# Kernel optimization log

Hardware: AMD Instinct MI355X
Metric: run time of the kernel (lower is better)

Reference implementation:

```python
import jax, jax.numpy as jnp
import numpy as np

B, C, P, T, H = 4, 256, 1024, 64, 8
D = C // H
SCALE = float(np.sqrt(D * T))


def setup_inputs() -> dict:
    key = jax.random.key(0)
    ks = jax.random.split(key, 7)
    s = 1.0 / np.sqrt(C)
    return {
        "x": jax.random.normal(ks[0], (B, C, P, T), dtype=jnp.float32),
        "Wk": jax.random.uniform(ks[1], (C, C), dtype=jnp.float32, minval=-s, maxval=s),
        "bk": jax.random.uniform(ks[2], (C,), dtype=jnp.float32, minval=-s, maxval=s),
        "Wq": jax.random.uniform(ks[3], (C, C), dtype=jnp.float32, minval=-s, maxval=s),
        "bq": jax.random.uniform(ks[4], (C,), dtype=jnp.float32, minval=-s, maxval=s),
        "Wv": jax.random.uniform(ks[5], (C, C), dtype=jnp.float32, minval=-s, maxval=s),
        "bv": jax.random.uniform(ks[6], (C,), dtype=jnp.float32, minval=-s, maxval=s),
    }


def _proj_split(x, W, b):
    # 1x1 conv == channel-mixing linear; then split heads: b (h d) p t -> b h d p t
    y = jnp.einsum('bcpt,oc->bopt', x, W) + b[None, :, None, None]
    Bs, _, Ps, Ts = y.shape
    return y.reshape(Bs, H, D, Ps, Ts)


def reference(x, Wk, bk, Wq, bq, Wv, bv):
    k = _proj_split(x, Wk, bk)
    q = _proj_split(x, Wq, bq)
    v = _proj_split(x, Wv, bv)
    # contract jointly over d and t
    energy = jnp.einsum('bhdpt,bhdqt->bhpq', k, q)
    attn = jax.nn.softmax(energy / SCALE, axis=-1)
    out = jnp.einsum('bhpq,bhdpt->bhdqt', attn, v)
    # merge heads: b h d q t -> b (h d) q t
    return out.reshape(B, C, P, T)
```

## Files before the change

kernel.cpp:

```cpp
#include <hip/hip_runtime.h>
#include <cstdint>
#include <cstddef>

#define NB 4
#define NC 256
#define NP 1024
#define NT 64
#define NH 8
#define ND 32
#define NF 2048
#define NPT 65536
#define KQV_ELEMS 67108864ull
#define INV_SCALE 0.022097086912079608f

typedef unsigned short u16;
typedef __bf16 bf16x8 __attribute__((ext_vector_type(8)));
typedef short  s16x8  __attribute__((ext_vector_type(8)));
typedef short  s16x4  __attribute__((ext_vector_type(4)));
typedef float  f32x4  __attribute__((ext_vector_type(4)));

__device__ __forceinline__ u16 f2bf(float f) {
  unsigned u = __builtin_bit_cast(unsigned, f);
  u += 0x7fffu + ((u >> 16) & 1u);
  return (u16)(u >> 16);
}
__device__ __forceinline__ float bf2f(u16 h) {
  unsigned u = ((unsigned)h) << 16;
  return __builtin_bit_cast(float, u);
}
__device__ __forceinline__ int swz(int row) { return ((row ^ (row >> 3)) & 7) << 4; }

#define GLOAD_LDS16(gp, lp) __builtin_amdgcn_global_load_lds( \
    (const __attribute__((address_space(1))) void*)(gp),      \
    (__attribute__((address_space(3))) void*)(lp), 16, 0, 0)

__device__ __forceinline__ f32x4 mfma16(bf16x8 a, bf16x8 b, f32x4 c) {
  return __builtin_amdgcn_mfma_f32_16x16x32_bf16(a, b, c, 0, 0, 0);
}

__global__ __launch_bounds__(256) void wcast_kernel(
    const float* __restrict__ Wk, const float* __restrict__ Wq,
    const float* __restrict__ Wv, u16* __restrict__ wbf)
{
  int pj = blockIdx.y;
  const float* W = (pj == 0) ? Wk : ((pj == 1) ? Wq : Wv);
  int idx = blockIdx.x * 1024 + threadIdx.x * 4;
  float4 v = *(const float4*)(W + idx);
  s16x4 pk;
  pk[0] = (short)f2bf(v.x); pk[1] = (short)f2bf(v.y);
  pk[2] = (short)f2bf(v.z); pk[3] = (short)f2bf(v.w);
  *(s16x4*)(wbf + (size_t)pj * 65536 + idx) = pk;
}

__global__ __launch_bounds__(256, 2) void xcast_kernel(
    const float* __restrict__ x, u16* __restrict__ xT)
{
  int ptt = blockIdx.x;
  int ct  = blockIdx.y;
  int b   = blockIdx.z;
  __shared__ __align__(16) u16 L[64 * 64];
  int tid = threadIdx.x;
#pragma unroll
  for (int i = 0; i < 4; i++) {
    int cl  = i * 16 + (tid >> 4);
    int ptl = (tid & 15) * 4;
    float4 v = *(const float4*)(x + ((size_t)(b * NC + ct * 64 + cl)) * NPT +
                                ptt * 64 + ptl);
    s16x4 pk;
    pk[0] = (short)f2bf(v.x); pk[1] = (short)f2bf(v.y);
    pk[2] = (short)f2bf(v.z); pk[3] = (short)f2bf(v.w);
    *(s16x4*)((char*)L + ((cl * 128 + ptl * 2) ^ swz(cl))) = pk;
  }
  __syncthreads();
#pragma unroll
  for (int i = 0; i < 2; i++) {
    int ptl = i * 32 + (tid >> 3);
    int c8  = (tid & 7) * 8;
    s16x8 v;
#pragma unroll
    for (int j = 0; j < 8; j++) {
      int row = c8 + j;
      v[j] = (short)*(const u16*)((char*)L + ((row * 128 + ptl * 2) ^ swz(row)));
    }
    *(s16x8*)(xT + ((size_t)b * NPT + (size_t)ptt * 64 + ptl) * NC + ct * 64 + c8) = v;
  }
}

template <int KT>
__device__ __forceinline__ void gemm_core(const u16* __restrict__ A,
                                          const u16* __restrict__ Bp,
                                          u16* As, u16* Bs, f32x4 acc[4][4])
{
  const int tid = threadIdx.x, lane = tid & 63, wave = tid >> 6;
  const int wm = (wave >> 1) * 64, wn = (wave & 1) * 64;
  for (int ks = 0; ks < KT / 64; ks++) {
    const int k0 = ks * 64;
    __syncthreads();
#pragma unroll
    for (int i = 0; i < 4; i++) {
      int r0 = wave * 32 + i * 8;
      int row = r0 + (lane >> 3);
      int col = k0 + (lane & 7) * 8;
      GLOAD_LDS16(A  + (size_t)row * KT + col, &As[r0 * 64]);
      GLOAD_LDS16(Bp + (size_t)row * KT + col, &Bs[r0 * 64]);
    }
    __syncthreads();
#pragma unroll
    for (int kk = 0; kk < 2; kk++) {
      bf16x8 af[4], bfr[4];
#pragma unroll
      for (int f = 0; f < 4; f++) {
        int ra = wm + f * 16 + (lane & 15);
        af[f]  = *(const bf16x8*)((char*)As + ra * 128 + kk * 64 + (lane >> 4) * 16);
        int rb = wn + f * 16 + (lane & 15);
        bfr[f] = *(const bf16x8*)((char*)Bs + rb * 128 + kk * 64 + (lane >> 4) * 16);
      }
#pragma unroll
      for (int fm = 0; fm < 4; fm++)
#pragma unroll
        for (int fn = 0; fn < 4; fn++)
          acc[fm][fn] = mfma16(af[fm], bfr[fn], acc[fm][fn]);
    }
  }
}

__global__ __launch_bounds__(256, 2) void proj_kernel(
    const u16* __restrict__ wbf, const u16* __restrict__ xT,
    const float* __restrict__ bk, const float* __restrict__ bq,
    const float* __restrict__ bv, u16* __restrict__ kqv)
{
  int d0 = blockIdx.x;
  int b  = blockIdx.y;
  int xcd = d0 & 7, r = d0 >> 3;
  int j = r % 6, tch = r / 6;
  int ptile = tch * 8 + xcd;
  int pj = j >> 1, mt = j & 1;
  const float* bias = (pj == 0) ? bk : ((pj == 1) ? bq : bv);
  u16* outb = kqv + (size_t)pj * KQV_ELEMS;

  const int m0 = mt * 128;
  const int n0 = ptile * 128;

  const u16* A  = wbf + (size_t)pj * 65536 + (size_t)m0 * NC;
  const u16* Bp = xT + ((size_t)b * NPT + (size_t)n0) * NC;

  __shared__ __align__(16) u16 As[128 * 64];
  __shared__ __align__(16) u16 Bs[128 * 64];

  f32x4 acc[4][4];
#pragma unroll
  for (int a = 0; a < 4; a++)
#pragma unroll
    for (int c = 0; c < 4; c++) acc[a][c] = (f32x4){0.f, 0.f, 0.f, 0.f};

  gemm_core<NC>(A, Bp, As, Bs, acc);

  const int lane = threadIdx.x & 63, wave = threadIdx.x >> 6;
  const int wm = (wave >> 1) * 64, wn = (wave & 1) * 64;
#pragma unroll
  for (int fm = 0; fm < 4; fm++) {
#pragma unroll
    for (int jj = 0; jj < 4; jj++) {
      int m = wm + fm * 16 + (lane >> 4) * 4 + jj;
      int o = m0 + m;
      float bsv = bias[o];
      int hh = o >> 5, dd = o & 31;
#pragma unroll
      for (int fn = 0; fn < 4; fn++) {
        int n = n0 + wn + fn * 16 + (lane & 15);
        int p = n >> 6, t = n & 63;
        outb[((size_t)(b * NH + hh) * NP + p) * NF + dd * 64 + t] =
            f2bf(acc[fm][fn][jj] + bsv);
      }
    }
  }
}

__global__ __launch_bounds__(256, 2) void transpose_kernel(
    const u16* __restrict__ in, u16* __restrict__ outp)
{
  int ft = blockIdx.x;
  int pt = blockIdx.y;
  int slab = blockIdx.z;
  __shared__ __align__(16) u16 L[64 * 64];
  int t = threadIdx.x;
  const u16* ip = in + (size_t)slab * NP * NF;
#pragma unroll
  for (int i = 0; i < 2; i++) {
    int pl = i * 32 + (t >> 3);
    int c8 = (t & 7) * 8;
    s16x8 v = *(const s16x8*)(ip + (size_t)(pt * 64 + pl) * NF + ft * 64 + c8);
    *(s16x8*)((char*)L + ((pl * 128 + c8 * 2) ^ swz(pl))) = v;
  }
  __syncthreads();
  u16* op = outp + (size_t)slab * NP * NF;
#pragma unroll
  for (int i = 0; i < 2; i++) {
    int fl = i * 32 + (t >> 3);
    int p8 = (t & 7) * 8;
    s16x8 v;
#pragma unroll
    for (int j2 = 0; j2 < 8; j2++) {
      int row = p8 + j2;
      v[j2] = (short)*(const u16*)((char*)L + ((row * 128 + fl * 2) ^ swz(row)));
    }
    *(s16x8*)(op + (size_t)(ft * 64 + fl) * NP + pt * 64 + p8) = v;
  }
}

#define STG1(TT, I, OP) do {                                                   \
    const u16* gp_ = (OP ? Bg : Ag) + (size_t)grow[I] * KT + (TT) * 32 + gcol[I]; \
    GLOAD_LDS16(gp_, L + ((((TT) & 3) * 32768 + (OP) * 16384 +                 \
                           ((I) & 1 ? W1 : W0)) >> 1));                        \
  } while (0)

#define FENCE() do {                                                           \
    asm volatile("" ::: "memory");                                             \
    __builtin_amdgcn_sched_barrier(0);                                         \
  } while (0)

#define KBODY(J, WAITASM, DOSTG) do {                                          \
    const int bufb_ = ((J) & 3) * 32768;                                       \
    bf16x8 a_[4], b_[4];                                                       \
    _Pragma("unroll")                                                          \
    for (int mf = 0; mf < 4; mf++)                                             \
      a_[mf] = *(const bf16x8*)((const char*)L + bufb_ + baseA + mf * 1024);   \
    _Pragma("unroll")                                                          \
    for (int nf = 0; nf < 4; nf++)                                             \
      b_[nf] = *(const bf16x8*)((const char*)L + bufb_ + baseB + nf * 1024);   \
    if (DOSTG) { STG1((J) + 3, 0, 0); STG1((J) + 3, 1, 0); }                   \
    __builtin_amdgcn_s_barrier();                                              \
    asm volatile("s_waitcnt lgkmcnt(0)" ::: "memory");                         \
    __builtin_amdgcn_sched_barrier(0);                                         \
    __builtin_amdgcn_s_setprio(1);                                             \
    _Pragma("unroll")                                                          \
    for (int mf = 0; mf < 4; mf++)                                             \
      _Pragma("unroll")                                                        \
      for (int nf = 0; nf < 4; nf++)                                           \
        acc[mf][nf] = mfma16(a_[mf], b_[nf], acc[mf][nf]);                     \
    __builtin_amdgcn_s_setprio(0);                                             \
    __builtin_amdgcn_sched_barrier(0);                                         \
    __builtin_amdgcn_s_barrier();                                              \
    FENCE();                                                                   \
    bf16x8 a2_[4];                                                             \
    _Pragma("unroll")                                                          \
    for (int mf = 0; mf < 4; mf++)                                             \
      a2_[mf] = *(const bf16x8*)((const char*)L + bufb_ + baseA +              \
                                 (4 + mf) * 1024);                             \
    if (DOSTG) { STG1((J) + 3, 2, 1); STG1((J) + 3, 3, 1); }                   \
    __builtin_amdgcn_s_barrier();                                              \
    asm volatile("s_waitcnt lgkmcnt(0)" ::: "memory");                         \
    __builtin_amdgcn_sched_barrier(0);                                         \
    __builtin_amdgcn_s_setprio(1);                                             \
    _Pragma("unroll")                                                          \
    for (int mf = 0; mf < 4; mf++)                                             \
      _Pragma("unroll")                                                        \
      for (int nf = 0; nf < 4; nf++)                                           \
        acc[4 + mf][nf] = mfma16(a2_[mf], b_[nf], acc[4 + mf][nf]);            \
    __builtin_amdgcn_s_setprio(0);                                             \
    __builtin_amdgcn_sched_barrier(0);                                         \
    asm volatile(WAITASM ::: "memory");                                        \
    __builtin_amdgcn_s_barrier();                                              \
    FENCE();                                                                   \
  } while (0)

template <int KT>
__device__ __forceinline__ void core256(const u16* __restrict__ Ag,
                                        const u16* __restrict__ Bg,
                                        u16* L, f32x4 acc[8][4])
{
  constexpr int NKT = KT / 32;
  const int tid  = threadIdx.x;
  const int lane = tid & 63;
  const int wv   = tid >> 6;
  const int wr = wv >> 2, wc = wv & 3;

  int grow[4], gcol[4];
#pragma unroll
  for (int i = 0; i < 4; i++) {
    int oi   = (tid + (i & 1) * 512) * 16;
    int loff = oi ^ (((oi >> 6) & 3) << 4);
    grow[i] = loff >> 6;
    gcol[i] = (loff & 63) >> 1;
  }
  const int W0 = wv * 1024;
  const int W1 = wv * 1024 + 8192;

  const int rowA  = wr * 128 + (lane & 15);
  const int baseA = rowA * 64 + (((lane >> 4) * 16) ^ ((rowA & 3) << 4));
  const int rowB  = wc * 64 + (lane & 15);
  const int baseB = 16384 + rowB * 64 + (((lane >> 4) * 16) ^ ((rowB & 3) << 4));

#pragma unroll
  for (int tt = 0; tt < 3; tt++) {
    STG1(tt, 0, 0); STG1(tt, 1, 0); STG1(tt, 2, 1); STG1(tt, 3, 1);
  }
  __builtin_amdgcn_sched_barrier(0);
  asm volatile("s_waitcnt vmcnt(8)" ::: "memory");
  __builtin_amdgcn_s_barrier();
  FENCE();

  for (int j = 0; j < NKT - 3; ++j)
    KBODY(j, "s_waitcnt vmcnt(8)", 1);
  KBODY(NKT - 3, "s_waitcnt vmcnt(4)", 0);
  KBODY(NKT - 2, "s_waitcnt vmcnt(0)", 0);
  KBODY(NKT - 1, "", 0);
}

__global__ __launch_bounds__(512, 2) void qk256_kernel(
    const u16* __restrict__ kb, const u16* __restrict__ qb, u16* __restrict__ S)
{
  extern __shared__ u16 L[];
  int bid = blockIdx.x;
  int xcd = bid & 7, r = bid >> 3;
  int bh  = xcd * 4 + (r >> 4);
  int til = r & 15;
  int mt  = til >> 2, nt = til & 3;

  const u16* Ag = qb + (size_t)bh * NP * NF + (size_t)mt * 256 * NF;
  const u16* Bg = kb + (size_t)bh * NP * NF + (size_t)nt * 256 * NF;

  f32x4 acc[8][4];
#pragma unroll
  for (int a = 0; a < 8; a++)
#pragma unroll
    for (int c = 0; c < 4; c++) acc[a][c] = (f32x4){0.f, 0.f, 0.f, 0.f};

  core256<NF>(Ag, Bg, L, acc);

  const int lane = threadIdx.x & 63, wv = threadIdx.x >> 6;
  const int wr = wv >> 2, wc = wv & 3;
  u16* Sp = S + (size_t)bh * NP * NP;
#pragma unroll
  for (int mf = 0; mf < 8; mf++)
#pragma unroll
    for (int jj = 0; jj < 4; jj++) {
      int m = mt * 256 + wr * 128 + mf * 16 + (lane >> 4) * 4 + jj;
#pragma unroll
      for (int nf = 0; nf < 4; nf++) {
        int n = nt * 256 + wc * 64 + nf * 16 + (lane & 15);
        Sp[(size_t)m * NP + n] = f2bf(acc[mf][nf][jj] * INV_SCALE);
      }
    }
}

__global__ __launch_bounds__(512, 2) void av256_kernel(
    const u16* __restrict__ Ab, const u16* __restrict__ Vt, float* __restrict__ out)
{
  extern __shared__ u16 L[];
  int bid = blockIdx.x;
  int xcd = bid & 7, r = bid >> 3;
  int bh  = xcd * 4 + (r >> 5);
  int til = r & 31;
  int mt  = til >> 3, ntf = til & 7;

  const u16* Ag = Ab + (size_t)bh * NP * NP + (size_t)mt * 256 * NP;
  const u16* Bg = Vt + (size_t)bh * NF * NP + (size_t)ntf * 256 * NP;

  f32x4 acc[8][4];
#pragma unroll
  for (int a = 0; a < 8; a++)
#pragma unroll
    for (int c = 0; c < 4; c++) acc[a][c] = (f32x4){0.f, 0.f, 0.f, 0.f};

  core256<NP>(Ag, Bg, L, acc);

  const int lane = threadIdx.x & 63, wv = threadIdx.x >> 6;
  const int wr = wv >> 2, wc = wv & 3;
  int b = bh >> 3, h = bh & 7;
#pragma unroll
  for (int mf = 0; mf < 8; mf++)
#pragma unroll
    for (int jj = 0; jj < 4; jj++) {
      int m = mt * 256 + wr * 128 + mf * 16 + (lane >> 4) * 4 + jj;
#pragma unroll
      for (int nf = 0; nf < 4; nf++) {
        int n = ntf * 256 + wc * 64 + nf * 16 + (lane & 15);
        int dd = n >> 6, t = n & 63;
        out[((size_t)(b * NC + h * ND + dd) * NP + m) * NT + t] = acc[mf][nf][jj];
      }
    }
}

__global__ __launch_bounds__(256, 2) void softmax_kernel(
    const u16* __restrict__ S, u16* __restrict__ A)
{
  int cb = blockIdx.x;
  int bh = blockIdx.y;
  int tid = threadIdx.x;
  int c  = tid & 63;
  int qs = tid >> 6;
  int col = cb * 64 + c;
  const u16* Sp = S + (size_t)bh * NP * NP + col;
  float m = -1e30f, l = 0.f;
  for (int q = qs * 256; q < qs * 256 + 256; q++) {
    float v = bf2f(Sp[(size_t)q * NP]);
    float mn = fmaxf(m, v);
    l = l * __expf(m - mn) + __expf(v - mn);
    m = mn;
  }
  __shared__ float ms[4][64], ls[4][64];
  ms[qs][c] = m; ls[qs][c] = l;
  __syncthreads();
  float M = fmaxf(fmaxf(ms[0][c], ms[1][c]), fmaxf(ms[2][c], ms[3][c]));
  float L = ls[0][c] * __expf(ms[0][c] - M) + ls[1][c] * __expf(ms[1][c] - M) +
            ls[2][c] * __expf(ms[2][c] - M) + ls[3][c] * __expf(ms[3][c] - M);
  float inv = 1.f / L;
  u16* Ap = A + (size_t)bh * NP * NP + col;
  for (int q = qs * 256; q < qs * 256 + 256; q++) {
    float v = bf2f(Sp[(size_t)q * NP]);
    Ap[(size_t)q * NP] = f2bf(__expf(v - M) * inv);
  }
}

extern "C" void kernel_launch(void* const* d_in, const int* in_sizes, int n_in,
                              void* d_out, int out_size, void* d_ws, size_t ws_size,
                              hipStream_t stream)
{
  if (ws_size < 4ull * KQV_ELEMS * sizeof(u16)) return;

  const float* x  = (const float*)d_in[0];
  const float* Wk = (const float*)d_in[1];
  const float* bk = (const float*)d_in[2];
  const float* Wq = (const float*)d_in[3];
  const float* bq = (const float*)d_in[4];
  const float* Wv = (const float*)d_in[5];
  const float* bv = (const float*)d_in[6];

  u16* kb = (u16*)d_ws;
  u16* qb = kb + KQV_ELEMS;
  u16* vb = kb + 2 * KQV_ELEMS;
  u16* vt = kb + 3 * KQV_ELEMS;

  u16* xT  = (u16*)d_out;
  u16* wbf = xT + KQV_ELEMS;
  u16* Sb  = xT + KQV_ELEMS + 262144;
  u16* Ab  = kb;

  (void)hipFuncSetAttribute((const void*)qk256_kernel,
                            hipFuncAttributeMaxDynamicSharedMemorySize, 131072);
  (void)hipFuncSetAttribute((const void*)av256_kernel,
                            hipFuncAttributeMaxDynamicSharedMemorySize, 131072);

  wcast_kernel<<<dim3(64, 3), 256, 0, stream>>>(Wk, Wq, Wv, wbf);
  xcast_kernel<<<dim3(1024, 4, 4), 256, 0, stream>>>(x, xT);
  proj_kernel<<<dim3(3072, 4), 256, 0, stream>>>(wbf, xT, bk, bq, bv, kb);
  transpose_kernel<<<dim3(32, 16, 32), 256, 0, stream>>>(vb, vt);
  qk256_kernel<<<dim3(512), 512, 131072, stream>>>(kb, qb, Sb);
  softmax_kernel<<<dim3(16, 32), 256, 0, stream>>>(Sb, Ab);
  av256_kernel<<<dim3(1024), 512, 131072, stream>>>(Ab, vt, (float*)d_out);
}
```

Baseline: 719.0 us.

## Stage projection epilogue through LDS and vectorize softmax column loads

The projection kernel's epilogue now writes bias-added bf16 results into the reused shared-memory tile and then emits 16-byte coalesced stores per head/row, replacing scattered 2-byte global stores. The column softmax now has each thread handle 8 adjacent columns with 16-byte vector loads and stores, with 8 row-slices per block and a 4x smaller grid. Both changes aim to cut uncoalesced memory traffic, at the cost of an extra LDS round trip and barrier, more registers in softmax, and fewer softmax blocks.

```diff
diff --git a/kernel.cpp b/kernel.cpp
--- a/kernel.cpp
+++ b/kernel.cpp
@@ -144,8 +144,7 @@
   const u16* A  = wbf + (size_t)pj * 65536 + (size_t)m0 * NC;
   const u16* Bp = xT + ((size_t)b * NPT + (size_t)n0) * NC;
 
-  __shared__ __align__(16) u16 As[128 * 64];
-  __shared__ __align__(16) u16 Bs[128 * 64];
+  __shared__ __align__(16) u16 SB[2][128 * 64];
 
   f32x4 acc[4][4];
 #pragma unroll
@@ -153,26 +152,37 @@
 #pragma unroll
     for (int c = 0; c < 4; c++) acc[a][c] = (f32x4){0.f, 0.f, 0.f, 0.f};
 
-  gemm_core<NC>(A, Bp, As, Bs, acc);
-
-  const int lane = threadIdx.x & 63, wave = threadIdx.x >> 6;
+  gemm_core<NC>(A, Bp, SB[0], SB[1], acc);
+
+  const int tid  = threadIdx.x;
+  const int lane = tid & 63, wave = tid >> 6;
   const int wm = (wave >> 1) * 64, wn = (wave & 1) * 64;
+
+  __syncthreads();
+  u16* Lt = &SB[0][0];
 #pragma unroll
   for (int fm = 0; fm < 4; fm++) {
 #pragma unroll
     for (int jj = 0; jj < 4; jj++) {
       int m = wm + fm * 16 + (lane >> 4) * 4 + jj;
-      int o = m0 + m;
-      float bsv = bias[o];
-      int hh = o >> 5, dd = o & 31;
+      float bsv = bias[m0 + m];
 #pragma unroll
       for (int fn = 0; fn < 4; fn++) {
-        int n = n0 + wn + fn * 16 + (lane & 15);
-        int p = n >> 6, t = n & 63;
-        outb[((size_t)(b * NH + hh) * NP + p) * NF + dd * 64 + t] =
-            f2bf(acc[fm][fn][jj] + bsv);
+        int n = wn + fn * 16 + (lane & 15);
+        Lt[m * 128 + n] = f2bf(acc[fm][fn][jj] + bsv);
       }
     }
+  }
+  __syncthreads();
+
+  const int p0 = ptile * 2;
+#pragma unroll
+  for (int i = 0; i < 8; i++) {
+    int hh = mt * 4 + (i >> 1);
+    int p  = p0 + (i & 1);
+    s16x8 v = *(const s16x8*)(Lt + ((i >> 1) * 32 + (tid >> 3)) * 128 +
+                              (i & 1) * 64 + (tid & 7) * 8);
+    *(s16x8*)(outb + ((size_t)(b * NH + hh) * NP + p) * NF + tid * 8) = v;
   }
 }
 
@@ -388,28 +398,51 @@
   int cb = blockIdx.x;
   int bh = blockIdx.y;
   int tid = threadIdx.x;
-  int c  = tid & 63;
-  int qs = tid >> 6;
-  int col = cb * 64 + c;
-  const u16* Sp = S + (size_t)bh * NP * NP + col;
-  float m = -1e30f, l = 0.f;
-  for (int q = qs * 256; q < qs * 256 + 256; q++) {
-    float v = bf2f(Sp[(size_t)q * NP]);
-    float mn = fmaxf(m, v);
-    l = l * __expf(m - mn) + __expf(v - mn);
-    m = mn;
-  }
-  __shared__ float ms[4][64], ls[4][64];
-  ms[qs][c] = m; ls[qs][c] = l;
+  int cg  = tid & 31;
+  int qs  = tid >> 5;
+  int col0 = cb * 256 + cg * 8;
+  const u16* Sp = S + (size_t)bh * NP * NP + col0;
+
+  float m[8], l[8];
+#pragma unroll
+  for (int j2 = 0; j2 < 8; j2++) { m[j2] = -1e30f; l[j2] = 0.f; }
+  for (int q = qs * 128; q < qs * 128 + 128; q++) {
+    s16x8 v = *(const s16x8*)(Sp + (size_t)q * NP);
+#pragma unroll
+    for (int j2 = 0; j2 < 8; j2++) {
+      float f = bf2f((u16)v[j2]);
+      float mn = fmaxf(m[j2], f);
+      l[j2] = l[j2] * __expf(m[j2] - mn) + __expf(f - mn);
+      m[j2] = mn;
+    }
+  }
+  __shared__ float ms[8][256], ls[8][256];
+#pragma unroll
+  for (int j2 = 0; j2 < 8; j2++) {
+    ms[qs][cg * 8 + j2] = m[j2];
+    ls[qs][cg * 8 + j2] = l[j2];
+  }
   __syncthreads();
-  float M = fmaxf(fmaxf(ms[0][c], ms[1][c]), fmaxf(ms[2][c], ms[3][c]));
-  float L = ls[0][c] * __expf(ms[0][c] - M) + ls[1][c] * __expf(ms[1][c] - M) +
-            ls[2][c] * __expf(ms[2][c] - M) + ls[3][c] * __expf(ms[3][c] - M);
-  float inv = 1.f / L;
-  u16* Ap = A + (size_t)bh * NP * NP + col;
-  for (int q = qs * 256; q < qs * 256 + 256; q++) {
-    float v = bf2f(Sp[(size_t)q * NP]);
-    Ap[(size_t)q * NP] = f2bf(__expf(v - M) * inv);
+  float M[8], Li[8];
+#pragma unroll
+  for (int j2 = 0; j2 < 8; j2++) {
+    int c = cg * 8 + j2;
+    float mm = ms[0][c];
+#pragma unroll
+    for (int k = 1; k < 8; k++) mm = fmaxf(mm, ms[k][c]);
+    float ll = 0.f;
+#pragma unroll
+    for (int k = 0; k < 8; k++) ll += ls[k][c] * __expf(ms[k][c] - mm);
+    M[j2] = mm; Li[j2] = 1.f / ll;
+  }
+  u16* Ap = A + (size_t)bh * NP * NP + col0;
+  for (int q = qs * 128; q < qs * 128 + 128; q++) {
+    s16x8 v = *(const s16x8*)(Sp + (size_t)q * NP);
+    s16x8 o;
+#pragma unroll
+    for (int j2 = 0; j2 < 8; j2++)
+      o[j2] = (short)f2bf(__expf(bf2f((u16)v[j2]) - M[j2]) * Li[j2]);
+    *(s16x8*)(Ap + (size_t)q * NP) = o;
   }
 }
 
@@ -447,6 +480,6 @@
   proj_kernel<<<dim3(3072, 4), 256, 0, stream>>>(wbf, xT, bk, bq, bv, kb);
   transpose_kernel<<<dim3(32, 16, 32), 256, 0, stream>>>(vb, vt);
   qk256_kernel<<<dim3(512), 512, 131072, stream>>>(kb, qb, Sb);
-  softmax_kernel<<<dim3(16, 32), 256, 0, stream>>>(Sb, Ab);
+  softmax_kernel<<<dim3(4, 32), 256, 0, stream>>>(Sb, Ab);
   av256_kernel<<<dim3(1024), 512, 131072, stream>>>(Ab, vt, (float*)d_out);
 }
```

After: 773.6 us. +7.6%, slower.
